# Kernel tuning notes

Measured on AMD Instinct MI355X. Metric: run time of the kernel, lower is better.

Reference implementation:

```python
import jax, jax.numpy as jnp
import numpy as np

GRID = (128, 128)
LR = 0.1
SIGMA = 3.0


def setup_inputs() -> dict:
    key = jax.random.key(0)
    k1, k2 = jax.random.split(key)
    x = jax.random.normal(k1, (4096, 256), dtype=jnp.float32)
    weights = jax.random.normal(k2, (128, 128, 256), dtype=jnp.float32)
    return {"x": x, "weights": weights}


def reference(x, weights):
    """One SOM training step: find BMU for each sample, then apply the
    Gaussian-neighborhood weight update (mean over the batch).
    Returns the updated weights [R, C, D]."""
    B, D = x.shape
    R, C, _ = weights.shape

    # ---- forward / find_bmu: squared distances x -> all neurons ----
    w_flat = weights.reshape(R * C, D)                     # [N, D]
    d2 = (jnp.sum(x * x, axis=1)[:, None]
          + jnp.sum(w_flat * w_flat, axis=1)[None, :]
          - 2.0 * x @ w_flat.T)                            # [B, N]
    bmu_idx = jnp.argmin(d2, axis=1)                       # [B]
    bmu_rows = bmu_idx // C                                # [B]
    bmu_cols = bmu_idx % C                                 # [B]

    # ---- update_weights: Gaussian neighborhood around each BMU ----
    rows = jnp.arange(R, dtype=jnp.float32)                # grid coords
    cols = jnp.arange(C, dtype=jnp.float32)
    dr2 = (rows[None, :] - bmu_rows[:, None].astype(jnp.float32)) ** 2  # [B, R]
    dc2 = (cols[None, :] - bmu_cols[:, None].astype(jnp.float32)) ** 2  # [B, C]
    neuron_dists = dr2[:, :, None] + dc2[:, None, :]       # [B, R, C]
    neigh = jnp.exp(-neuron_dists / (2.0 * SIGMA ** 2))    # [B, R, C]

    # mean_b lr*neigh[b,r,c]*(x[b,d] - w[r,c,d])  without a [B,R,C,D] tensor
    num = jnp.einsum('brc,bd->rcd', neigh, x)              # [R, C, D]
    neigh_sum = jnp.sum(neigh, axis=0)                     # [R, C]
    delta_mean = (LR / B) * (num - neigh_sum[:, :, None] * weights)
    return weights + delta_mean
```

## Files before the change

### kernel.cpp

```cpp
#include <hip/hip_runtime.h>

typedef _Float16 f16;
typedef _Float16 f16x8 __attribute__((ext_vector_type(8)));
typedef _Float16 f16x4 __attribute__((ext_vector_type(4)));
typedef float f32x4 __attribute__((ext_vector_type(4)));

#define GLL(gp, lp) __builtin_amdgcn_global_load_lds( \
    (const __attribute__((address_space(1))) void*)(gp), \
    (__attribute__((address_space(3))) void*)(lp), 16, 0, 0)

__global__ void prep_w_kernel(const float* __restrict__ w, f16* __restrict__ whi,
                              f16* __restrict__ wlo, float* __restrict__ wnorm) {
    int wv = blockIdx.x * 4 + (threadIdx.x >> 6);
    int lane = threadIdx.x & 63;
    float4 v = reinterpret_cast<const float4*>(w + (size_t)wv * 256)[lane];
    float vv[4] = {v.x, v.y, v.z, v.w};
    f16x4 h, l;
    float ss = 0.f;
#pragma unroll
    for (int i = 0; i < 4; i++) {
        f16 hh = (f16)vv[i];
        h[i] = hh;
        l[i] = (f16)(vv[i] - (float)hh);
        ss += vv[i] * vv[i];
    }
    *(f16x4*)(whi + (size_t)wv * 256 + lane * 4) = h;
    *(f16x4*)(wlo + (size_t)wv * 256 + lane * 4) = l;
#pragma unroll
    for (int off = 32; off > 0; off >>= 1) ss += __shfl_down(ss, off);
    if (lane == 0) wnorm[wv] = ss;
}

__global__ void prep_x_kernel(const float* __restrict__ x, f16* __restrict__ xhi,
                              f16* __restrict__ xlo, f16* __restrict__ xT,
                              unsigned long long* __restrict__ bmu) {
    __shared__ f16 tile[64][72];
    const int b0 = blockIdx.x * 64;
    const int d0 = blockIdx.y * 64;
    const int t = threadIdx.x;
    if (blockIdx.y == 0 && blockIdx.x < 16) bmu[blockIdx.x * 256 + t] = ~0ull;
    const int lb = t >> 2, dq = t & 3;
    const float* src = x + (size_t)(b0 + lb) * 256 + d0 + dq * 16;
    f16x8 h[2], l[2];
#pragma unroll
    for (int q = 0; q < 4; q++) {
        float4 v = reinterpret_cast<const float4*>(src)[q];
        float vv[4] = {v.x, v.y, v.z, v.w};
#pragma unroll
        for (int i = 0; i < 4; i++) {
            int idx = q * 4 + i;
            f16 hh = (f16)vv[i];
            h[idx >> 3][idx & 7] = hh;
            l[idx >> 3][idx & 7] = (f16)(vv[i] - (float)hh);
        }
    }
    f16* dh = xhi + (size_t)(b0 + lb) * 256 + d0 + dq * 16;
    f16* dl = xlo + (size_t)(b0 + lb) * 256 + d0 + dq * 16;
    *(f16x8*)dh = h[0]; *(f16x8*)(dh + 8) = h[1];
    *(f16x8*)dl = l[0]; *(f16x8*)(dl + 8) = l[1];
#pragma unroll
    for (int i = 0; i < 16; i++) tile[lb][dq * 16 + i] = (i < 8) ? h[0][i] : h[1][i - 8];
    __syncthreads();
    const int dlc = t >> 2, bq = t & 3;
    f16x8 o[2];
#pragma unroll
    for (int i = 0; i < 16; i++) o[i >> 3][i & 7] = tile[bq * 16 + i][dlc];
    f16* dst = xT + (size_t)(d0 + dlc) * 4096 + b0 + bq * 16;
    *(f16x8*)dst = o[0]; *(f16x8*)(dst + 8) = o[1];
}

__launch_bounds__(256, 2)
__global__ void gemm_argmin_kernel(const f16* __restrict__ xhi, const f16* __restrict__ xlo,
                                   const f16* __restrict__ whi, const f16* __restrict__ wlo,
                                   const float* __restrict__ wnorm,
                                   unsigned long long* __restrict__ bmu) {
    __shared__ f16 As[128][64];
    __shared__ f16 Bs[128][64];
    __shared__ float s_wn[128];
    const int m0 = blockIdx.x * 128;
    const int n0 = blockIdx.y * 128;
    const int tid = threadIdx.x;
    const int lane = tid & 63, wid = tid >> 6;
    const int wm = wid >> 1, wn = wid & 1;
    const int l15 = lane & 15, l4 = lane >> 4;
    if (tid < 128) s_wn[tid] = wnorm[n0 + tid];
    f32x4 acc[4][4] = {};
    for (int kt = 0; kt < 768; kt += 64) {
        const f16* asrc = (kt >= 512) ? xlo : xhi;
        const f16* bsrc = (kt >= 256 && kt < 512) ? wlo : whi;
        const int kk = kt & 255;
        __syncthreads();
#pragma unroll
        for (int q = 0; q < 4; q++) {
            int off = tid * 16 + q * 4096;
            int row = off >> 7;
            int colh = (off & 127) >> 1;
            GLL(asrc + (size_t)(m0 + row) * 256 + kk + colh, (char*)(&As[0][0]) + off);
        }
#pragma unroll
        for (int q = 0; q < 4; q++) {
            int off = tid * 16 + q * 4096;
            int row = off >> 7;
            int colh = (off & 127) >> 1;
            GLL(bsrc + (size_t)(n0 + row) * 256 + kk + colh, (char*)(&Bs[0][0]) + off);
        }
        __syncthreads();
#pragma unroll
        for (int ks = 0; ks < 2; ks++) {
            f16x8 af[4], bf[4];
#pragma unroll
            for (int i = 0; i < 4; i++)
                af[i] = *(const f16x8*)&As[wm * 64 + i * 16 + l15][ks * 32 + l4 * 8];
#pragma unroll
            for (int i = 0; i < 4; i++)
                bf[i] = *(const f16x8*)&Bs[wn * 64 + i * 16 + l15][ks * 32 + l4 * 8];
#pragma unroll
            for (int i = 0; i < 4; i++)
#pragma unroll
                for (int j = 0; j < 4; j++)
                    acc[i][j] = __builtin_amdgcn_mfma_f32_16x16x32_f16(af[i], bf[j], acc[i][j], 0, 0, 0);
        }
    }
#pragma unroll
    for (int mi = 0; mi < 4; mi++) {
#pragma unroll
        for (int j = 0; j < 4; j++) {
            float best = 1e30f;
            int bidx = 0x7fffffff;
#pragma unroll
            for (int ni = 0; ni < 4; ni++) {
                int nl = wn * 64 + ni * 16 + l15;
                float v = s_wn[nl] - 2.0f * acc[mi][ni][j];
                int g = n0 + nl;
                if (v < best || (v == best && g < bidx)) { best = v; bidx = g; }
            }
#pragma unroll
            for (int off = 1; off < 16; off <<= 1) {
                float ov = __shfl_xor(best, off);
                int oi = __shfl_xor(bidx, off);
                if (ov < best || (ov == best && oi < bidx)) { best = ov; bidx = oi; }
            }
            if (l15 == 0) {
                unsigned u = __float_as_uint(best);
                u = (u & 0x80000000u) ? ~u : (u | 0x80000000u);
                unsigned long long key = ((unsigned long long)u << 32) | (unsigned)bidx;
                int m = m0 + wm * 64 + mi * 16 + l4 * 4 + j;
                atomicMin(&bmu[m], key);
            }
        }
    }
}

__global__ void tables_kernel(const unsigned long long* __restrict__ bmu,
                              f16* __restrict__ erT, f16* __restrict__ ecT,
                              float* __restrict__ ns) {
    __shared__ float gauss[128];
    const int tid = threadIdx.x;
    const int gb = blockIdx.x * 256 + tid;
    if (tid < 128) gauss[tid] = expf(-(float)(tid * tid) / 18.0f);
#pragma unroll
    for (int i = 0; i < 4; i++) ns[blockIdx.x * 1024 + tid * 4 + i] = 0.0f;
    __syncthreads();
    const int n = (int)(bmu[gb] & 0xffffffffull);
    const int br = n >> 7, bc = n & 127;
    for (int p = 0; p < 128; p++) {
        int dr = p - br; if (dr < 0) dr = -dr;
        int dc = p - bc; if (dc < 0) dc = -dc;
        erT[(size_t)p * 4096 + gb] = (f16)gauss[dr];
        ecT[(size_t)p * 4096 + gb] = (f16)gauss[dc];
    }
}

__global__ void neigh_sum_kernel(const f16* __restrict__ erT, const f16* __restrict__ ecT,
                                 float* __restrict__ ns) {
    const int r = blockIdx.x, chunk = blockIdx.y;
    const int c = threadIdx.x;
    const f16* erp = erT + (size_t)r * 4096 + chunk * 512;
    const f16* ecp = ecT + (size_t)c * 4096 + chunk * 512;
    float acc = 0.f;
    for (int b = 0; b < 512; b += 8) {
        f16x8 ev = *(const f16x8*)(erp + b);
        f16x8 cv = *(const f16x8*)(ecp + b);
#pragma unroll
        for (int i = 0; i < 8; i++) acc += (float)ev[i] * (float)cv[i];
    }
    atomicAdd(&ns[r * 128 + c], acc);
}

__launch_bounds__(256, 2)
__global__ void gemm_update_kernel(const f16* __restrict__ xT, const f16* __restrict__ erT,
                                   const f16* __restrict__ ecT, const float* __restrict__ w,
                                   const float* __restrict__ ns, float* __restrict__ out) {
    __shared__ f16 As[64][64];
    __shared__ f16 Bs[128][64];
    __shared__ float s_ns[64];
    const int n0 = blockIdx.x * 64;
    const int d0 = blockIdx.y * 128;
    const int r0 = n0 >> 7;
    const int c0 = n0 & 127;
    const int tid = threadIdx.x;
    const int lane = tid & 63, wid = tid >> 6;
    const int wm = wid >> 1, wn = wid & 1;
    const int l15 = lane & 15, l4 = lane >> 4;
    if (tid < 64) s_ns[tid] = ns[n0 + tid];
    f32x4 acc[2][4] = {};
    const int cc = tid >> 2;
    const int k0 = (tid & 3) * 16;
    const f16* erow = erT + (size_t)r0 * 4096;
    const f16* ecrow = ecT + (size_t)(c0 + cc) * 4096;
    for (int kt = 0; kt < 4096; kt += 64) {
        __syncthreads();
#pragma unroll
        for (int q = 0; q < 4; q++) {
            int off = tid * 16 + q * 4096;
            int row = off >> 7;
            int colh = (off & 127) >> 1;
            GLL(xT + (size_t)(d0 + row) * 4096 + kt + colh, (char*)(&Bs[0][0]) + off);
        }
        f16x8 e0 = *(const f16x8*)(erow + kt + k0);
        f16x8 e1 = *(const f16x8*)(erow + kt + k0 + 8);
        f16x8 g0 = *(const f16x8*)(ecrow + kt + k0);
        f16x8 g1 = *(const f16x8*)(ecrow + kt + k0 + 8);
        *(f16x8*)&As[cc][k0] = e0 * g0;
        *(f16x8*)&As[cc][k0 + 8] = e1 * g1;
        __syncthreads();
#pragma unroll
        for (int ks = 0; ks < 2; ks++) {
            f16x8 af[2], bf[4];
#pragma unroll
            for (int i = 0; i < 2; i++)
                af[i] = *(const f16x8*)&As[wm * 32 + i * 16 + l15][ks * 32 + l4 * 8];
#pragma unroll
            for (int i = 0; i < 4; i++)
                bf[i] = *(const f16x8*)&Bs[wn * 64 + i * 16 + l15][ks * 32 + l4 * 8];
#pragma unroll
            for (int i = 0; i < 2; i++)
#pragma unroll
                for (int j = 0; j < 4; j++)
                    acc[i][j] = __builtin_amdgcn_mfma_f32_16x16x32_f16(af[i], bf[j], acc[i][j], 0, 0, 0);
        }
    }
    const float s = 0.1f / 4096.0f;
#pragma unroll
    for (int mi = 0; mi < 2; mi++) {
#pragma unroll
        for (int ni = 0; ni < 4; ni++) {
#pragma unroll
            for (int j = 0; j < 4; j++) {
                int nloc = wm * 32 + mi * 16 + l4 * 4 + j;
                int dloc = wn * 64 + ni * 16 + l15;
                size_t gi = (size_t)(n0 + nloc) * 256 + d0 + dloc;
                float wv = w[gi];
                out[gi] = wv + s * (acc[mi][ni][j] - s_ns[nloc] * wv);
            }
        }
    }
}

extern "C" void kernel_launch(void* const* d_in, const int* in_sizes, int n_in,
                              void* d_out, int out_size, void* d_ws, size_t ws_size,
                              hipStream_t stream) {
    const float* x = (const float*)d_in[0];
    const float* w = (const float*)d_in[1];
    float* out = (float*)d_out;
    char* ws = (char*)d_ws;

    f16* whi = (f16*)(ws + 0);
    f16* wlo = (f16*)(ws + 8388608);
    f16* xhi = (f16*)(ws + 16777216);
    f16* xlo = (f16*)(ws + 18874368);
    f16* xT  = (f16*)(ws + 20971520);
    f16* erT = (f16*)(ws + 23068672);
    f16* ecT = (f16*)(ws + 24117248);
    float* wnorm = (float*)(ws + 25165824);
    float* ns    = (float*)(ws + 25231360);
    unsigned long long* bmu = (unsigned long long*)(ws + 25296896);

    prep_w_kernel<<<4096, 256, 0, stream>>>(w, whi, wlo, wnorm);
    prep_x_kernel<<<dim3(64, 4), 256, 0, stream>>>(x, xhi, xlo, xT, bmu);
    gemm_argmin_kernel<<<dim3(32, 128), 256, 0, stream>>>(xhi, xlo, whi, wlo, wnorm, bmu);
    tables_kernel<<<16, 256, 0, stream>>>(bmu, erT, ecT, ns);
    neigh_sum_kernel<<<dim3(128, 8), 128, 0, stream>>>(erT, ecT, ns);
    gemm_update_kernel<<<dim3(256, 2), 256, 0, stream>>>(xT, erT, ecT, w, ns, out);
}
```

Before: 351.0 us.

## Replace neighborhood GEMM with BMU scatter plus separable Gaussian convolutions

Rather than building per-sample Gaussian row and column tables and running a 4096-deep GEMM for the update, each sample is scatter-added into a per-neuron sum and count grid. Separable 1D Gaussian convolutions along rows and then columns give the numerator and the neighbor sums. The transpose in prep_x is dropped, and the argmin GEMM gains an XOR swizzle on its LDS tiles plus a higher occupancy bound. This cuts the update cost to an O(N·D·(R+C)) convolution in fp32, at the price of float atomics whose order is nondeterministic.

```diff
diff --git a/kernel.cpp b/kernel.cpp
--- a/kernel.cpp
+++ b/kernel.cpp
@@ -32,44 +32,23 @@
 }
 
 __global__ void prep_x_kernel(const float* __restrict__ x, f16* __restrict__ xhi,
-                              f16* __restrict__ xlo, f16* __restrict__ xT,
-                              unsigned long long* __restrict__ bmu) {
-    __shared__ f16 tile[64][72];
-    const int b0 = blockIdx.x * 64;
-    const int d0 = blockIdx.y * 64;
-    const int t = threadIdx.x;
-    if (blockIdx.y == 0 && blockIdx.x < 16) bmu[blockIdx.x * 256 + t] = ~0ull;
-    const int lb = t >> 2, dq = t & 3;
-    const float* src = x + (size_t)(b0 + lb) * 256 + d0 + dq * 16;
-    f16x8 h[2], l[2];
-#pragma unroll
-    for (int q = 0; q < 4; q++) {
-        float4 v = reinterpret_cast<const float4*>(src)[q];
-        float vv[4] = {v.x, v.y, v.z, v.w};
-#pragma unroll
-        for (int i = 0; i < 4; i++) {
-            int idx = q * 4 + i;
-            f16 hh = (f16)vv[i];
-            h[idx >> 3][idx & 7] = hh;
-            l[idx >> 3][idx & 7] = (f16)(vv[i] - (float)hh);
-        }
-    }
-    f16* dh = xhi + (size_t)(b0 + lb) * 256 + d0 + dq * 16;
-    f16* dl = xlo + (size_t)(b0 + lb) * 256 + d0 + dq * 16;
-    *(f16x8*)dh = h[0]; *(f16x8*)(dh + 8) = h[1];
-    *(f16x8*)dl = l[0]; *(f16x8*)(dl + 8) = l[1];
-#pragma unroll
-    for (int i = 0; i < 16; i++) tile[lb][dq * 16 + i] = (i < 8) ? h[0][i] : h[1][i - 8];
-    __syncthreads();
-    const int dlc = t >> 2, bq = t & 3;
-    f16x8 o[2];
-#pragma unroll
-    for (int i = 0; i < 16; i++) o[i >> 3][i & 7] = tile[bq * 16 + i][dlc];
-    f16* dst = xT + (size_t)(d0 + dlc) * 4096 + b0 + bq * 16;
-    *(f16x8*)dst = o[0]; *(f16x8*)(dst + 8) = o[1];
-}
-
-__launch_bounds__(256, 2)
+                              f16* __restrict__ xlo, unsigned long long* __restrict__ bmu) {
+    const int t = blockIdx.x * 256 + threadIdx.x;
+    if (blockIdx.x < 16) bmu[blockIdx.x * 256 + threadIdx.x] = ~0ull;
+    float4 v = reinterpret_cast<const float4*>(x)[t];
+    float vv[4] = {v.x, v.y, v.z, v.w};
+    f16x4 h, l;
+#pragma unroll
+    for (int i = 0; i < 4; i++) {
+        f16 hh = (f16)vv[i];
+        h[i] = hh;
+        l[i] = (f16)(vv[i] - (float)hh);
+    }
+    *(f16x4*)(xhi + (size_t)t * 4) = h;
+    *(f16x4*)(xlo + (size_t)t * 4) = l;
+}
+
+__launch_bounds__(256, 4)
 __global__ void gemm_argmin_kernel(const f16* __restrict__ xhi, const f16* __restrict__ xlo,
                                    const f16* __restrict__ whi, const f16* __restrict__ wlo,
                                    const float* __restrict__ wnorm,
@@ -83,6 +62,7 @@
     const int lane = tid & 63, wid = tid >> 6;
     const int wm = wid >> 1, wn = wid & 1;
     const int l15 = lane & 15, l4 = lane >> 4;
+    const int swz = (l15 & 7) << 3;
     if (tid < 128) s_wn[tid] = wnorm[n0 + tid];
     f32x4 acc[4][4] = {};
     for (int kt = 0; kt < 768; kt += 64) {
@@ -94,14 +74,14 @@
         for (int q = 0; q < 4; q++) {
             int off = tid * 16 + q * 4096;
             int row = off >> 7;
-            int colh = (off & 127) >> 1;
+            int colh = ((off & 127) ^ ((row & 7) << 4)) >> 1;
             GLL(asrc + (size_t)(m0 + row) * 256 + kk + colh, (char*)(&As[0][0]) + off);
         }
 #pragma unroll
         for (int q = 0; q < 4; q++) {
             int off = tid * 16 + q * 4096;
             int row = off >> 7;
-            int colh = (off & 127) >> 1;
+            int colh = ((off & 127) ^ ((row & 7) << 4)) >> 1;
             GLL(bsrc + (size_t)(n0 + row) * 256 + kk + colh, (char*)(&Bs[0][0]) + off);
         }
         __syncthreads();
@@ -110,10 +90,10 @@
             f16x8 af[4], bf[4];
 #pragma unroll
             for (int i = 0; i < 4; i++)
-                af[i] = *(const f16x8*)&As[wm * 64 + i * 16 + l15][ks * 32 + l4 * 8];
+                af[i] = *(const f16x8*)&As[wm * 64 + i * 16 + l15][(ks * 32 + l4 * 8) ^ swz];
 #pragma unroll
             for (int i = 0; i < 4; i++)
-                bf[i] = *(const f16x8*)&Bs[wn * 64 + i * 16 + l15][ks * 32 + l4 * 8];
+                bf[i] = *(const f16x8*)&Bs[wn * 64 + i * 16 + l15][(ks * 32 + l4 * 8) ^ swz];
 #pragma unroll
             for (int i = 0; i < 4; i++)
 #pragma unroll
@@ -151,109 +131,118 @@
     }
 }
 
-__global__ void tables_kernel(const unsigned long long* __restrict__ bmu,
-                              f16* __restrict__ erT, f16* __restrict__ ecT,
-                              float* __restrict__ ns) {
-    __shared__ float gauss[128];
+__global__ void zeroS_kernel(float4* __restrict__ S4, float4* __restrict__ count4) {
+    const int t = blockIdx.x * 256 + threadIdx.x;
+    S4[t] = float4{0.f, 0.f, 0.f, 0.f};
+    if (blockIdx.x < 16) count4[t] = float4{0.f, 0.f, 0.f, 0.f};
+}
+
+__global__ void scatter_kernel(const float* __restrict__ x,
+                               const unsigned long long* __restrict__ bmu,
+                               float* __restrict__ S, float* __restrict__ count) {
+    const int b = blockIdx.x * 4 + (threadIdx.x >> 6);
+    const int lane = threadIdx.x & 63;
+    const int n = (int)(bmu[b] & 0xffffffffull);
+    float4 v = reinterpret_cast<const float4*>(x + (size_t)b * 256)[lane];
+    float* dst = S + (size_t)n * 256 + lane * 4;
+    atomicAdd(dst + 0, v.x);
+    atomicAdd(dst + 1, v.y);
+    atomicAdd(dst + 2, v.z);
+    atomicAdd(dst + 3, v.w);
+    if (lane == 0) atomicAdd(count + n, 1.0f);
+}
+
+__global__ void ns_pass1_kernel(const float* __restrict__ count, float* __restrict__ cnt_r) {
+    __shared__ float g[128];
+    const int r = blockIdx.x;
+    const int bc = threadIdx.x;
+    g[bc] = expf(-(float)(bc * bc) / 18.0f);
+    __syncthreads();
+    float acc = 0.f;
+    for (int br = 0; br < 128; br++) {
+        int dd = br - r; dd = dd < 0 ? -dd : dd;
+        acc += g[dd] * count[br * 128 + bc];
+    }
+    cnt_r[r * 128 + bc] = acc;
+}
+
+__global__ void conv_r_kernel(const float* __restrict__ S, float* __restrict__ T1, int h) {
+    __shared__ float tile[128][64];
+    __shared__ float g[128];
     const int tid = threadIdx.x;
-    const int gb = blockIdx.x * 256 + tid;
-    if (tid < 128) gauss[tid] = expf(-(float)(tid * tid) / 18.0f);
-#pragma unroll
-    for (int i = 0; i < 4; i++) ns[blockIdx.x * 1024 + tid * 4 + i] = 0.0f;
-    __syncthreads();
-    const int n = (int)(bmu[gb] & 0xffffffffull);
-    const int br = n >> 7, bc = n & 127;
-    for (int p = 0; p < 128; p++) {
-        int dr = p - br; if (dr < 0) dr = -dr;
-        int dc = p - bc; if (dc < 0) dc = -dc;
-        erT[(size_t)p * 4096 + gb] = (f16)gauss[dr];
-        ecT[(size_t)p * 4096 + gb] = (f16)gauss[dc];
-    }
-}
-
-__global__ void neigh_sum_kernel(const f16* __restrict__ erT, const f16* __restrict__ ecT,
-                                 float* __restrict__ ns) {
-    const int r = blockIdx.x, chunk = blockIdx.y;
-    const int c = threadIdx.x;
-    const f16* erp = erT + (size_t)r * 4096 + chunk * 512;
-    const f16* ecp = ecT + (size_t)c * 4096 + chunk * 512;
-    float acc = 0.f;
-    for (int b = 0; b < 512; b += 8) {
-        f16x8 ev = *(const f16x8*)(erp + b);
-        f16x8 cv = *(const f16x8*)(ecp + b);
-#pragma unroll
-        for (int i = 0; i < 8; i++) acc += (float)ev[i] * (float)cv[i];
-    }
-    atomicAdd(&ns[r * 128 + c], acc);
-}
-
-__launch_bounds__(256, 2)
-__global__ void gemm_update_kernel(const f16* __restrict__ xT, const f16* __restrict__ erT,
-                                   const f16* __restrict__ ecT, const float* __restrict__ w,
-                                   const float* __restrict__ ns, float* __restrict__ out) {
-    __shared__ f16 As[64][64];
-    __shared__ f16 Bs[128][64];
-    __shared__ float s_ns[64];
-    const int n0 = blockIdx.x * 64;
-    const int d0 = blockIdx.y * 128;
-    const int r0 = n0 >> 7;
-    const int c0 = n0 & 127;
+    const int j0 = blockIdx.x * 64;
+    if (tid < 128) g[tid] = expf(-(float)(tid * tid) / 18.0f);
+    const int jbase = (j0 >> 7) * 256 + h * 128 + (j0 & 127);
+#pragma unroll
+    for (int q = 0; q < 8; q++) {
+        int off = tid * 16 + q * 4096;
+        int row = off >> 8;
+        int col = (off & 255) >> 2;
+        GLL(S + (size_t)row * 32768 + jbase + col, (char*)(&tile[0][0]) + off);
+    }
+    __syncthreads();
+    const int jg = (tid & 15) * 4;
+    const int r0 = (tid >> 4) * 8;
+    f32x4 acc[8] = {};
+    for (int br = 0; br < 128; br++) {
+        f32x4 v = *(const f32x4*)&tile[br][jg];
+#pragma unroll
+        for (int i = 0; i < 8; i++) {
+            int dd = br - (r0 + i); dd = dd < 0 ? -dd : dd;
+            acc[i] += g[dd] * v;
+        }
+    }
+#pragma unroll
+    for (int i = 0; i < 8; i++)
+        *(f32x4*)&T1[(size_t)(r0 + i) * 16384 + j0 + jg] = acc[i];
+}
+
+__global__ void conv_c_kernel(const float* __restrict__ T1, const float* __restrict__ cnt_r,
+                              const float* __restrict__ w, float* __restrict__ out, int h) {
+    __shared__ float tile[128][64];
+    __shared__ float g[128];
+    __shared__ float s_cnt[128];
+    __shared__ float s_ns[128];
     const int tid = threadIdx.x;
-    const int lane = tid & 63, wid = tid >> 6;
-    const int wm = wid >> 1, wn = wid & 1;
-    const int l15 = lane & 15, l4 = lane >> 4;
-    if (tid < 64) s_ns[tid] = ns[n0 + tid];
-    f32x4 acc[2][4] = {};
-    const int cc = tid >> 2;
-    const int k0 = (tid & 3) * 16;
-    const f16* erow = erT + (size_t)r0 * 4096;
-    const f16* ecrow = ecT + (size_t)(c0 + cc) * 4096;
-    for (int kt = 0; kt < 4096; kt += 64) {
-        __syncthreads();
-#pragma unroll
-        for (int q = 0; q < 4; q++) {
-            int off = tid * 16 + q * 4096;
-            int row = off >> 7;
-            int colh = (off & 127) >> 1;
-            GLL(xT + (size_t)(d0 + row) * 4096 + kt + colh, (char*)(&Bs[0][0]) + off);
-        }
-        f16x8 e0 = *(const f16x8*)(erow + kt + k0);
-        f16x8 e1 = *(const f16x8*)(erow + kt + k0 + 8);
-        f16x8 g0 = *(const f16x8*)(ecrow + kt + k0);
-        f16x8 g1 = *(const f16x8*)(ecrow + kt + k0 + 8);
-        *(f16x8*)&As[cc][k0] = e0 * g0;
-        *(f16x8*)&As[cc][k0 + 8] = e1 * g1;
-        __syncthreads();
-#pragma unroll
-        for (int ks = 0; ks < 2; ks++) {
-            f16x8 af[2], bf[4];
-#pragma unroll
-            for (int i = 0; i < 2; i++)
-                af[i] = *(const f16x8*)&As[wm * 32 + i * 16 + l15][ks * 32 + l4 * 8];
-#pragma unroll
-            for (int i = 0; i < 4; i++)
-                bf[i] = *(const f16x8*)&Bs[wn * 64 + i * 16 + l15][ks * 32 + l4 * 8];
-#pragma unroll
-            for (int i = 0; i < 2; i++)
-#pragma unroll
-                for (int j = 0; j < 4; j++)
-                    acc[i][j] = __builtin_amdgcn_mfma_f32_16x16x32_f16(af[i], bf[j], acc[i][j], 0, 0, 0);
+    const int r = blockIdx.x;
+    const int d0 = blockIdx.y * 64;
+    if (tid < 128) g[tid] = expf(-(float)(tid * tid) / 18.0f);
+    if (tid >= 128 && tid < 256) s_cnt[tid - 128] = cnt_r[r * 128 + (tid - 128)];
+#pragma unroll
+    for (int q = 0; q < 8; q++) {
+        int off = tid * 16 + q * 4096;
+        int row = off >> 8;
+        int col = (off & 255) >> 2;
+        GLL(T1 + (size_t)r * 16384 + (size_t)row * 128 + d0 + col, (char*)(&tile[0][0]) + off);
+    }
+    __syncthreads();
+    if (tid < 128) {
+        float acc = 0.f;
+        for (int bc = 0; bc < 128; bc++) {
+            int dd = tid - bc; dd = dd < 0 ? -dd : dd;
+            acc += g[dd] * s_cnt[bc];
+        }
+        s_ns[tid] = acc;
+    }
+    __syncthreads();
+    const int jg = (tid & 15) * 4;
+    const int c0 = (tid >> 4) * 8;
+    f32x4 acc[8] = {};
+    for (int bc = 0; bc < 128; bc++) {
+        f32x4 v = *(const f32x4*)&tile[bc][jg];
+#pragma unroll
+        for (int i = 0; i < 8; i++) {
+            int dd = bc - (c0 + i); dd = dd < 0 ? -dd : dd;
+            acc[i] += g[dd] * v;
         }
     }
     const float s = 0.1f / 4096.0f;
 #pragma unroll
-    for (int mi = 0; mi < 2; mi++) {
-#pragma unroll
-        for (int ni = 0; ni < 4; ni++) {
-#pragma unroll
-            for (int j = 0; j < 4; j++) {
-                int nloc = wm * 32 + mi * 16 + l4 * 4 + j;
-                int dloc = wn * 64 + ni * 16 + l15;
-                size_t gi = (size_t)(n0 + nloc) * 256 + d0 + dloc;
-                float wv = w[gi];
-                out[gi] = wv + s * (acc[mi][ni][j] - s_ns[nloc] * wv);
-            }
-        }
+    for (int i = 0; i < 8; i++) {
+        size_t gi = ((size_t)(r * 128 + c0 + i)) * 256 + h * 128 + d0 + jg;
+        f32x4 wv = *(const f32x4*)&w[gi];
+        f32x4 o = wv + s * (acc[i] - s_ns[c0 + i] * wv);
+        *(f32x4*)&out[gi] = o;
     }
 }
 
@@ -267,19 +256,23 @@
 
     f16* whi = (f16*)(ws + 0);
     f16* wlo = (f16*)(ws + 8388608);
+    float* S = (float*)(ws + 0);
     f16* xhi = (f16*)(ws + 16777216);
     f16* xlo = (f16*)(ws + 18874368);
-    f16* xT  = (f16*)(ws + 20971520);
-    f16* erT = (f16*)(ws + 23068672);
-    f16* ecT = (f16*)(ws + 24117248);
-    float* wnorm = (float*)(ws + 25165824);
-    float* ns    = (float*)(ws + 25231360);
-    unsigned long long* bmu = (unsigned long long*)(ws + 25296896);
+    float* wnorm = (float*)(ws + 20971520);
+    float* T1 = (float*)(ws + 16777216);
+    unsigned long long* bmu = (unsigned long long*)(ws + 25165824);
+    float* count = (float*)(ws + 25198592);
+    float* cnt_r = (float*)(ws + 25264128);
 
     prep_w_kernel<<<4096, 256, 0, stream>>>(w, whi, wlo, wnorm);
-    prep_x_kernel<<<dim3(64, 4), 256, 0, stream>>>(x, xhi, xlo, xT, bmu);
+    prep_x_kernel<<<1024, 256, 0, stream>>>(x, xhi, xlo, bmu);
     gemm_argmin_kernel<<<dim3(32, 128), 256, 0, stream>>>(xhi, xlo, whi, wlo, wnorm, bmu);
-    tables_kernel<<<16, 256, 0, stream>>>(bmu, erT, ecT, ns);
-    neigh_sum_kernel<<<dim3(128, 8), 128, 0, stream>>>(erT, ecT, ns);
-    gemm_update_kernel<<<dim3(256, 2), 256, 0, stream>>>(xT, erT, ecT, w, ns, out);
-}
+    zeroS_kernel<<<4096, 256, 0, stream>>>((float4*)S, (float4*)count);
+    scatter_kernel<<<1024, 256, 0, stream>>>(x, bmu, S, count);
+    ns_pass1_kernel<<<128, 128, 0, stream>>>(count, cnt_r);
+    conv_r_kernel<<<256, 256, 0, stream>>>(S, T1, 0);
+    conv_c_kernel<<<dim3(128, 2), 256, 0, stream>>>(T1, cnt_r, w, out, 0);
+    conv_r_kernel<<<256, 256, 0, stream>>>(S, T1, 1);
+    conv_c_kernel<<<dim3(128, 2), 256, 0, stream>>>(T1, cnt_r, w, out, 1);
+}
```

Result: faster. 306.2 us (-12.8%).
